# Kernel tuning notes

Measured on AMD Instinct MI355X. Metric: run time of the kernel, lower is better.

The kernel has to match this reference:

```python
import jax, jax.numpy as jnp
import numpy as np

N_NODES = 100000
N_EDGES = 3200000
D_FEAT = 256
FILTERS = 256


def setup_inputs() -> dict:
    key = jax.random.key(0)
    k1, k2, k3, k4, k5 = jax.random.split(key, 5)
    x = jax.random.normal(k1, (N_NODES, D_FEAT), dtype=jnp.float32)
    edge_row = jax.random.randint(k2, (N_EDGES,), 0, N_NODES, dtype=jnp.int32)
    edge_col = jax.random.randint(k3, (N_EDGES,), 0, N_NODES, dtype=jnp.int32)
    edge_vals = jnp.ones((N_EDGES,), dtype=jnp.float32)
    w = jax.random.normal(k4, (D_FEAT, FILTERS), dtype=jnp.float32) * (2.0 / D_FEAT) ** 0.5  # he_normal
    b = jax.random.normal(k5, (FILTERS,), dtype=jnp.float32) * 0.05
    return {"x": x, "edge_row": edge_row, "edge_col": edge_col,
            "edge_vals": edge_vals, "w": w, "b": b}


def reference(x, edge_row, edge_col, edge_vals, w, b):
    n = x.shape[0]
    # normalize_A: D = rowsum(A); L = D^{-1/2} A D^{-1/2}
    deg = jax.ops.segment_sum(edge_vals, edge_row, num_segments=n)
    dinv = jnp.where(deg > 0, deg ** -0.5, 0.0)  # [N]
    norm_vals = edge_vals * dinv[edge_row] * dinv[edge_col]  # [E]
    # dense projection then sparse aggregation + bias + relu
    h = x @ w  # [N, F]
    msg = norm_vals[:, None] * h[edge_col]  # [E, F] gather + scale
    agg = jax.ops.segment_sum(msg, edge_row, num_segments=n)  # [N, F]
    return jax.nn.relu(agg + b)
```

## Files before the change

### kernel.cpp

```cpp
#include <hip/hip_runtime.h>
#include <hip/hip_bf16.h>


#define DF   256
#define RSH  7
#define RPB  128
#define CAP  4800
#define CHUNK 8192
#define LSTR 40

typedef __attribute__((ext_vector_type(8))) short short8;
typedef __attribute__((ext_vector_type(4))) float f32x4;

__device__ __forceinline__ unsigned short f2bf(float f) {
    unsigned int u = __float_as_uint(f);
    unsigned int r = (u + 0x7fffu + ((u >> 16) & 1u)) >> 16;
    return (unsigned short)r;
}
__device__ __forceinline__ unsigned int pack2(float a, float b) {
    unsigned int r;
    asm("v_cvt_pk_bf16_f32 %0, %1, %2" : "=v"(r) : "v"(a), "v"(b));
    return r;
}
__device__ __forceinline__ float bflo(unsigned int u) { return __uint_as_float(u << 16); }
__device__ __forceinline__ float bfhi(unsigned int u) { return __uint_as_float(u & 0xffff0000u); }

__global__ __launch_bounds__(256) void bhist_kernel(const int* __restrict__ row,
                                                    int* __restrict__ bh1, int NB, int NBLK, int E) {
    __shared__ int hist[1024];
    int t = threadIdx.x;
    for (int i = t; i < NB; i += 256) hist[i] = 0;
    __syncthreads();
    int base = blockIdx.x * CHUNK;
    int end = base + CHUNK; if (end > E) end = E;
    for (int i = base + t; i < end; i += 256)
        atomicAdd(&hist[row[i] >> RSH], 1);
    __syncthreads();
    for (int i = t; i < NB; i += 256)
        bh1[(size_t)i * NBLK + blockIdx.x] = hist[i];
}

__global__ __launch_bounds__(256) void bscan_kernel(const int* __restrict__ bh1,
                                                    int* __restrict__ bh2,
                                                    int* __restrict__ buckettot, int NB, int NBLK) {
    __shared__ int ps[256];
    int b = blockIdx.x, t = threadIdx.x;
    int e0 = 2 * t, e1 = 2 * t + 1;
    int v0 = (e0 < NBLK) ? bh1[(size_t)b * NBLK + e0] : 0;
    int v1 = (e1 < NBLK) ? bh1[(size_t)b * NBLK + e1] : 0;
    int tsum = v0 + v1;
    ps[t] = tsum;
    __syncthreads();
    for (int off = 1; off < 256; off <<= 1) {
        int v = (t >= off) ? ps[t - off] : 0;
        __syncthreads();
        ps[t] += v;
        __syncthreads();
    }
    int pre = ps[t] - tsum;
    if (e0 < NBLK) bh2[(size_t)e0 * NB + b] = pre;
    if (e1 < NBLK) bh2[(size_t)e1 * NB + b] = pre + v0;
    if (t == 255) buckettot[b] = ps[255];
}

__global__ __launch_bounds__(1024) void btot_kernel(const int* __restrict__ buckettot,
                                                    int* __restrict__ bucket_base, int NB) {
    __shared__ int ps[1024];
    int t = threadIdx.x;
    int v = (t < NB) ? buckettot[t] : 0;
    ps[t] = v;
    __syncthreads();
    for (int off = 1; off < 1024; off <<= 1) {
        int u = (t >= off) ? ps[t - off] : 0;
        __syncthreads();
        ps[t] += u;
        __syncthreads();
    }
    if (t < NB) bucket_base[t] = ps[t] - v;
    if (t == 1023) bucket_base[NB] = ps[1023];
}

__global__ __launch_bounds__(512) void bsort_kernel(const int* __restrict__ row,
                                                    const int* __restrict__ col,
                                                    const float* __restrict__ vals,
                                                    const int* __restrict__ bh2,
                                                    const int* __restrict__ bucket_base,
                                                    int2* __restrict__ bedge, int NB, int E) {
    __shared__ int2 sedge[CHUNK];
    __shared__ unsigned short sbkt[CHUNK];
    __shared__ int lhist[1024];
    __shared__ int lscan[1024];
    __shared__ int lbase[1024];
    __shared__ int ps[512];
    int t = threadIdx.x, blk = blockIdx.x;
    int base = blk * CHUNK;
    int end = base + CHUNK; if (end > E) end = E;
    int n = end - base;
    for (int i = t; i < NB; i += 512) {
        lhist[i] = 0;
        lbase[i] = bucket_base[i] + bh2[(size_t)blk * NB + i];
    }
    __syncthreads();
    for (int i = base + t; i < end; i += 512)
        atomicAdd(&lhist[row[i] >> RSH], 1);
    __syncthreads();
    int e0 = 2 * t, e1 = 2 * t + 1;
    int v0 = (e0 < NB) ? lhist[e0] : 0;
    int v1 = (e1 < NB) ? lhist[e1] : 0;
    int tsum = v0 + v1;
    ps[t] = tsum;
    __syncthreads();
    for (int off = 1; off < 512; off <<= 1) {
        int v = (t >= off) ? ps[t - off] : 0;
        __syncthreads();
        ps[t] += v;
        __syncthreads();
    }
    int pre = ps[t] - tsum;
    if (e0 < NB) lscan[e0] = pre;
    if (e1 < NB) lscan[e1] = pre + v0;
    __syncthreads();
    for (int i = t; i < NB; i += 512) lhist[i] = 0;
    __syncthreads();
    for (int i = base + t; i < end; i += 512) {
        int r = row[i];
        int b = r >> RSH;
        int p = atomicAdd(&lhist[b], 1);
        int slot = lscan[b] + p;
        sedge[slot] = make_int2(((r & (RPB - 1)) << 17) | col[i], __float_as_int(vals[i]));
        sbkt[slot] = (unsigned short)b;
    }
    __syncthreads();
    for (int i = t; i < n; i += 512) {
        int b = sbkt[i];
        bedge[lbase[b] + (i - lscan[b])] = sedge[i];
    }
}

__global__ __launch_bounds__(256) void deg_kernel(const int2* __restrict__ bedge,
                                                  const int* __restrict__ bucket_base,
                                                  float* __restrict__ dinv, int N) {
    __shared__ float acc[RPB];
    int b = blockIdx.x, t = threadIdx.x;
    if (t < RPB) acc[t] = 0.f;
    __syncthreads();
    int s = bucket_base[b], e = bucket_base[b + 1];
    for (int i = s + t; i < e; i += 256) {
        int2 ed = bedge[i];
        atomicAdd(&acc[ed.x >> 17], __int_as_float(ed.y));
    }
    __syncthreads();
    if (t < RPB) {
        int r = b * RPB + t;
        if (r < N) {
            float d = acc[t];
            dinv[r] = (d > 0.f) ? (1.0f / sqrtf(d)) : 0.f;
        }
    }
}

__global__ __launch_bounds__(256) void transpose_kernel(const float* __restrict__ w,
                                                        float* __restrict__ wT) {
    __shared__ float tile[32][33];
    int bx = blockIdx.x * 32, by = blockIdx.y * 32;
    int tx = threadIdx.x, ty = threadIdx.y;
    for (int j = ty; j < 32; j += 8) tile[j][tx] = w[(by + j) * DF + bx + tx];
    __syncthreads();
    for (int j = ty; j < 32; j += 8) wT[(bx + j) * DF + by + tx] = tile[tx][j];
}

__global__ __launch_bounds__(256, 2) void gemm_kernel(const float* __restrict__ x,
                                                      const float* __restrict__ wT,
                                                      const float* __restrict__ dinv,
                                                      unsigned short* __restrict__ h, int N) {
    __shared__ unsigned short Al[128 * LSTR];
    __shared__ unsigned short Bl[256 * LSTR];
    int tid = threadIdx.x;
    int by = blockIdx.x;
    int wv = tid >> 6, lane = tid & 63;
    int wr = wv >> 1, wc = wv & 1;
    int q = lane >> 4, mi = lane & 15;

    f32x4 acc[4][8];
#pragma unroll
    for (int i = 0; i < 4; ++i)
#pragma unroll
        for (int j = 0; j < 8; ++j) acc[i][j] = (f32x4){0.f, 0.f, 0.f, 0.f};

    int srow = tid >> 1;
    int sseg = (tid & 1) * 16;
    int axrow = by * 128 + srow; if (axrow >= N) axrow = N - 1;
    const float* ax = x + (long)axrow * DF + sseg;
    const float* bxp = wT + (long)tid * DF;
    unsigned short* Aw = &Al[srow * LSTR + sseg];
    unsigned short* Bw = &Bl[tid * LSTR];

    for (int kk = 0; kk < DF; kk += 32) {
        float4 a0 = *(const float4*)(ax + kk);
        float4 a1 = *(const float4*)(ax + kk + 4);
        float4 a2 = *(const float4*)(ax + kk + 8);
        float4 a3 = *(const float4*)(ax + kk + 12);
        float4 b0 = *(const float4*)(bxp + kk);
        float4 b1 = *(const float4*)(bxp + kk + 4);
        float4 b2 = *(const float4*)(bxp + kk + 8);
        float4 b3 = *(const float4*)(bxp + kk + 12);
        float4 b4 = *(const float4*)(bxp + kk + 16);
        float4 b5 = *(const float4*)(bxp + kk + 20);
        float4 b6 = *(const float4*)(bxp + kk + 24);
        float4 b7 = *(const float4*)(bxp + kk + 28);
        __syncthreads();
        uint4 pa;
        pa.x = pack2(a0.x, a0.y); pa.y = pack2(a0.z, a0.w);
        pa.z = pack2(a1.x, a1.y); pa.w = pack2(a1.z, a1.w);
        *(uint4*)Aw = pa;
        pa.x = pack2(a2.x, a2.y); pa.y = pack2(a2.z, a2.w);
        pa.z = pack2(a3.x, a3.y); pa.w = pack2(a3.z, a3.w);
        *(uint4*)(Aw + 8) = pa;
        uint4 pb;
        pb.x = pack2(b0.x, b0.y); pb.y = pack2(b0.z, b0.w);
        pb.z = pack2(b1.x, b1.y); pb.w = pack2(b1.z, b1.w);
        *(uint4*)Bw = pb;
        pb.x = pack2(b2.x, b2.y); pb.y = pack2(b2.z, b2.w);
        pb.z = pack2(b3.x, b3.y); pb.w = pack2(b3.z, b3.w);
        *(uint4*)(Bw + 8) = pb;
        pb.x = pack2(b4.x, b4.y); pb.y = pack2(b4.z, b4.w);
        pb.z = pack2(b5.x, b5.y); pb.w = pack2(b5.z, b5.w);
        *(uint4*)(Bw + 16) = pb;
        pb.x = pack2(b6.x, b6.y); pb.y = pack2(b6.z, b6.w);
        pb.z = pack2(b7.x, b7.y); pb.w = pack2(b7.z, b7.w);
        *(uint4*)(Bw + 24) = pb;
        __syncthreads();

        short8 af[4];
#pragma unroll
        for (int i = 0; i < 4; ++i)
            af[i] = *(const short8*)&Al[(wr * 64 + i * 16 + mi) * LSTR + q * 8];
#pragma unroll
        for (int j = 0; j < 8; ++j) {
            short8 bfj = *(const short8*)&Bl[(wc * 128 + j * 16 + mi) * LSTR + q * 8];
#pragma unroll
            for (int i = 0; i < 4; ++i)
                acc[i][j] = __builtin_amdgcn_mfma_f32_16x16x32_bf16(af[i], bfj, acc[i][j], 0, 0, 0);
        }
    }

#pragma unroll
    for (int i = 0; i < 4; ++i) {
        int base_row = by * 128 + wr * 64 + i * 16 + q * 4;
#pragma unroll
        for (int r = 0; r < 4; ++r) {
            int rg = base_row + r;
            if (rg < N) {
                float dv = dinv[rg];
#pragma unroll
                for (int j = 0; j < 8; ++j) {
                    int cg = wc * 128 + j * 16 + mi;
                    h[(long)rg * DF + cg] = f2bf(dv * acc[i][j][r]);
                }
            }
        }
    }
}

__global__ __launch_bounds__(256) void aggb_kernel(const unsigned short* __restrict__ h,
                                                   const int2* __restrict__ bedge,
                                                   const int* __restrict__ bucket_base,
                                                   const float* __restrict__ dinv,
                                                   const float* __restrict__ bias,
                                                   float* __restrict__ out, int N) {
    __shared__ int2 ledge[CAP];
    __shared__ int cnt[RPB];
    __shared__ int lrs[RPB + 1];
    __shared__ int lfill[RPB];
    int b = blockIdx.x, t = threadIdx.x;
    int s = bucket_base[b], e = bucket_base[b + 1];
    int tot = e - s;
    int cap_end = s + (tot < CAP ? tot : CAP);
    if (t < RPB) { cnt[t] = 0; lfill[t] = 0; }
    __syncthreads();
    for (int i = s + t; i < cap_end; i += 256)
        atomicAdd(&cnt[bedge[i].x >> 17], 1);
    __syncthreads();
    int myc = 0;
    if (t < RPB) { myc = cnt[t]; lrs[t] = myc; }
    __syncthreads();
    for (int off = 1; off < RPB; off <<= 1) {
        int v = (t < RPB && t >= off) ? lrs[t - off] : 0;
        __syncthreads();
        if (t < RPB) lrs[t] += v;
        __syncthreads();
    }
    if (t < RPB) {
        int iv = lrs[t];
        lrs[t] = iv - myc;
        if (t == RPB - 1) lrs[RPB] = iv;
    }
    __syncthreads();
    for (int i = s + t; i < cap_end; i += 256) {
        int2 ed = bedge[i];
        int rl = ed.x >> 17;
        int p = lrs[rl] + atomicAdd(&lfill[rl], 1);
        ledge[p] = make_int2(ed.x & 0x1FFFF, ed.y);
    }
    __syncthreads();
    int wv = t >> 6, lane = t & 63;
    int half = lane >> 5;
    int fl = (lane & 31) * 8;
    const unsigned short* hp = h + fl;
    for (int lr = wv; lr < RPB; lr += 4) {
        int r = b * RPB + lr;
        if (r >= N) break;
        int rs = lrs[lr], re = lrs[lr + 1];
        float a0 = 0, a1 = 0, a2 = 0, a3 = 0, a4 = 0, a5 = 0, a6 = 0, a7 = 0;
        int i = rs + half;
        for (; i + 6 < re; i += 8) {
            int2 e0 = ledge[i], e1 = ledge[i + 2], e2 = ledge[i + 4], e3 = ledge[i + 6];
            uint4 u0 = *(const uint4*)(hp + (long)e0.x * DF);
            uint4 u1 = *(const uint4*)(hp + (long)e1.x * DF);
            uint4 u2 = *(const uint4*)(hp + (long)e2.x * DF);
            uint4 u3 = *(const uint4*)(hp + (long)e3.x * DF);
            float v0 = __int_as_float(e0.y), v1 = __int_as_float(e1.y);
            float v2 = __int_as_float(e2.y), v3 = __int_as_float(e3.y);
            a0 += v0 * bflo(u0.x) + v1 * bflo(u1.x) + v2 * bflo(u2.x) + v3 * bflo(u3.x);
            a1 += v0 * bfhi(u0.x) + v1 * bfhi(u1.x) + v2 * bfhi(u2.x) + v3 * bfhi(u3.x);
            a2 += v0 * bflo(u0.y) + v1 * bflo(u1.y) + v2 * bflo(u2.y) + v3 * bflo(u3.y);
            a3 += v0 * bfhi(u0.y) + v1 * bfhi(u1.y) + v2 * bfhi(u2.y) + v3 * bfhi(u3.y);
            a4 += v0 * bflo(u0.z) + v1 * bflo(u1.z) + v2 * bflo(u2.z) + v3 * bflo(u3.z);
            a5 += v0 * bfhi(u0.z) + v1 * bfhi(u1.z) + v2 * bfhi(u2.z) + v3 * bfhi(u3.z);
            a6 += v0 * bflo(u0.w) + v1 * bflo(u1.w) + v2 * bflo(u2.w) + v3 * bflo(u3.w);
            a7 += v0 * bfhi(u0.w) + v1 * bfhi(u1.w) + v2 * bfhi(u2.w) + v3 * bfhi(u3.w);
        }
        for (; i < re; i += 2) {
            int2 e0 = ledge[i];
            float v0 = __int_as_float(e0.y);
            uint4 u0 = *(const uint4*)(hp + (long)e0.x * DF);
            a0 += v0 * bflo(u0.x); a1 += v0 * bfhi(u0.x);
            a2 += v0 * bflo(u0.y); a3 += v0 * bfhi(u0.y);
            a4 += v0 * bflo(u0.z); a5 += v0 * bfhi(u0.z);
            a6 += v0 * bflo(u0.w); a7 += v0 * bfhi(u0.w);
        }
        for (int j = cap_end + half; j < e; j += 2) {
            int2 ed = bedge[j];
            if ((ed.x >> 17) == lr) {
                float v0 = __int_as_float(ed.y);
                uint4 u0 = *(const uint4*)(hp + (long)(ed.x & 0x1FFFF) * DF);
                a0 += v0 * bflo(u0.x); a1 += v0 * bfhi(u0.x);
                a2 += v0 * bflo(u0.y); a3 += v0 * bfhi(u0.y);
                a4 += v0 * bflo(u0.z); a5 += v0 * bfhi(u0.z);
                a6 += v0 * bflo(u0.w); a7 += v0 * bfhi(u0.w);
            }
        }
        a0 += __shfl_xor(a0, 32); a1 += __shfl_xor(a1, 32);
        a2 += __shfl_xor(a2, 32); a3 += __shfl_xor(a3, 32);
        a4 += __shfl_xor(a4, 32); a5 += __shfl_xor(a5, 32);
        a6 += __shfl_xor(a6, 32); a7 += __shfl_xor(a7, 32);
        if (half == 0) {
            float dr = dinv[r];
            float4 b0 = *(const float4*)(bias + fl);
            float4 b1 = *(const float4*)(bias + fl + 4);
            float4 o0, o1;
            o0.x = fmaxf(fmaf(dr, a0, b0.x), 0.f);
            o0.y = fmaxf(fmaf(dr, a1, b0.y), 0.f);
            o0.z = fmaxf(fmaf(dr, a2, b0.z), 0.f);
            o0.w = fmaxf(fmaf(dr, a3, b0.w), 0.f);
            o1.x = fmaxf(fmaf(dr, a4, b1.x), 0.f);
            o1.y = fmaxf(fmaf(dr, a5, b1.y), 0.f);
            o1.z = fmaxf(fmaf(dr, a6, b1.z), 0.f);
            o1.w = fmaxf(fmaf(dr, a7, b1.w), 0.f);
            *(float4*)(out + (long)r * DF + fl) = o0;
            *(float4*)(out + (long)r * DF + fl + 4) = o1;
        }
    }
}

extern "C" void kernel_launch(void* const* d_in, const int* in_sizes, int n_in,
                              void* d_out, int out_size, void* d_ws, size_t ws_size,
                              hipStream_t stream) {
    const float* x   = (const float*)d_in[0];
    const int* erow  = (const int*)d_in[1];
    const int* ecol  = (const int*)d_in[2];
    const float* ev  = (const float*)d_in[3];
    const float* w   = (const float*)d_in[4];
    const float* b   = (const float*)d_in[5];
    float* out = (float*)d_out;

    int N = in_sizes[0] / DF;
    int E = in_sizes[1];
    int NB = (N + RPB - 1) >> RSH;
    int NBLK = (E + CHUNK - 1) / CHUNK;

    char* ws = (char*)d_ws;
    size_t Ea8 = (((size_t)E * 8) + 255) & ~(size_t)255;
    size_t Hs  = (((size_t)N * DF * 2) + 255) & ~(size_t)255;
    size_t Na  = (((size_t)N * 4) + 255) & ~(size_t)255;

    int2* bedge = (int2*)ws;
    char* reg2 = ws + Ea8;
    unsigned short* h = (unsigned short*)reg2;
    int* bh1 = (int*)reg2;
    int* bh2 = bh1 + (size_t)NB * NBLK;
    char* reg3 = reg2 + Hs;
    float* wT = (float*)reg3;
    float* dinv = (float*)(reg3 + 262144);
    int* buckettot = (int*)(reg3 + 262144 + Na);
    int* bucket_base = (int*)(reg3 + 262144 + Na + 8192);

    bhist_kernel<<<NBLK, 256, 0, stream>>>(erow, bh1, NB, NBLK, E);
    bscan_kernel<<<NB, 256, 0, stream>>>(bh1, bh2, buckettot, NB, NBLK);
    btot_kernel<<<1, 1024, 0, stream>>>(buckettot, bucket_base, NB);
    bsort_kernel<<<NBLK, 512, 0, stream>>>(erow, ecol, ev, bh2, bucket_base, bedge, NB, E);
    deg_kernel<<<NB, 256, 0, stream>>>(bedge, bucket_base, dinv, N);
    transpose_kernel<<<dim3(8, 8), dim3(32, 8), 0, stream>>>(w, wT);
    gemm_kernel<<<dim3((N + 127) / 128), 256, 0, stream>>>(x, wT, dinv, h, N);
    aggb_kernel<<<NB, 256, 0, stream>>>(h, bedge, bucket_base, dinv, b, out, N);
}
```

Before: 590.7 us.

## Load GEMM operands directly into MFMA registers, pre-convert weights to bf16

The transpose kernel now writes the weight matrix as bf16, and the GEMM drops its LDS staging. Each lane loads its MFMA fragments straight from global memory and prefetches the next K-slice of x in registers. This removes the LDS writes and reads and both per-iteration barriers. In exchange, the x rows are loaded in a less coalesced pattern, and each wave reloads its weight fragments from L2/L1 rather than sharing them through LDS, which may raise cache traffic and register pressure.

```diff
diff --git a/kernel.cpp b/kernel.cpp
--- a/kernel.cpp
+++ b/kernel.cpp
@@ -7,7 +7,6 @@
 #define RPB  128
 #define CAP  4800
 #define CHUNK 8192
-#define LSTR 40
 
 typedef __attribute__((ext_vector_type(8))) short short8;
 typedef __attribute__((ext_vector_type(4))) float f32x4;
@@ -160,21 +159,19 @@
 }
 
 __global__ __launch_bounds__(256) void transpose_kernel(const float* __restrict__ w,
-                                                        float* __restrict__ wT) {
+                                                        unsigned short* __restrict__ wbT) {
     __shared__ float tile[32][33];
     int bx = blockIdx.x * 32, by = blockIdx.y * 32;
     int tx = threadIdx.x, ty = threadIdx.y;
     for (int j = ty; j < 32; j += 8) tile[j][tx] = w[(by + j) * DF + bx + tx];
     __syncthreads();
-    for (int j = ty; j < 32; j += 8) wT[(bx + j) * DF + by + tx] = tile[tx][j];
+    for (int j = ty; j < 32; j += 8) wbT[(bx + j) * DF + by + tx] = f2bf(tile[tx][j]);
 }
 
 __global__ __launch_bounds__(256, 2) void gemm_kernel(const float* __restrict__ x,
-                                                      const float* __restrict__ wT,
+                                                      const unsigned short* __restrict__ wbT,
                                                       const float* __restrict__ dinv,
                                                       unsigned short* __restrict__ h, int N) {
-    __shared__ unsigned short Al[128 * LSTR];
-    __shared__ unsigned short Bl[256 * LSTR];
     int tid = threadIdx.x;
     int by = blockIdx.x;
     int wv = tid >> 6, lane = tid & 63;
@@ -187,60 +184,64 @@
 #pragma unroll
         for (int j = 0; j < 8; ++j) acc[i][j] = (f32x4){0.f, 0.f, 0.f, 0.f};
 
-    int srow = tid >> 1;
-    int sseg = (tid & 1) * 16;
-    int axrow = by * 128 + srow; if (axrow >= N) axrow = N - 1;
-    const float* ax = x + (long)axrow * DF + sseg;
-    const float* bxp = wT + (long)tid * DF;
-    unsigned short* Aw = &Al[srow * LSTR + sseg];
-    unsigned short* Bw = &Bl[tid * LSTR];
-
-    for (int kk = 0; kk < DF; kk += 32) {
-        float4 a0 = *(const float4*)(ax + kk);
-        float4 a1 = *(const float4*)(ax + kk + 4);
-        float4 a2 = *(const float4*)(ax + kk + 8);
-        float4 a3 = *(const float4*)(ax + kk + 12);
-        float4 b0 = *(const float4*)(bxp + kk);
-        float4 b1 = *(const float4*)(bxp + kk + 4);
-        float4 b2 = *(const float4*)(bxp + kk + 8);
-        float4 b3 = *(const float4*)(bxp + kk + 12);
-        float4 b4 = *(const float4*)(bxp + kk + 16);
-        float4 b5 = *(const float4*)(bxp + kk + 20);
-        float4 b6 = *(const float4*)(bxp + kk + 24);
-        float4 b7 = *(const float4*)(bxp + kk + 28);
-        __syncthreads();
-        uint4 pa;
-        pa.x = pack2(a0.x, a0.y); pa.y = pack2(a0.z, a0.w);
-        pa.z = pack2(a1.x, a1.y); pa.w = pack2(a1.z, a1.w);
-        *(uint4*)Aw = pa;
-        pa.x = pack2(a2.x, a2.y); pa.y = pack2(a2.z, a2.w);
-        pa.z = pack2(a3.x, a3.y); pa.w = pack2(a3.z, a3.w);
-        *(uint4*)(Aw + 8) = pa;
-        uint4 pb;
-        pb.x = pack2(b0.x, b0.y); pb.y = pack2(b0.z, b0.w);
-        pb.z = pack2(b1.x, b1.y); pb.w = pack2(b1.z, b1.w);
-        *(uint4*)Bw = pb;
-        pb.x = pack2(b2.x, b2.y); pb.y = pack2(b2.z, b2.w);
-        pb.z = pack2(b3.x, b3.y); pb.w = pack2(b3.z, b3.w);
-        *(uint4*)(Bw + 8) = pb;
-        pb.x = pack2(b4.x, b4.y); pb.y = pack2(b4.z, b4.w);
-        pb.z = pack2(b5.x, b5.y); pb.w = pack2(b5.z, b5.w);
-        *(uint4*)(Bw + 16) = pb;
-        pb.x = pack2(b6.x, b6.y); pb.y = pack2(b6.z, b6.w);
-        pb.z = pack2(b7.x, b7.y); pb.w = pack2(b7.z, b7.w);
-        *(uint4*)(Bw + 24) = pb;
-        __syncthreads();
-
-        short8 af[4];
-#pragma unroll
-        for (int i = 0; i < 4; ++i)
-            af[i] = *(const short8*)&Al[(wr * 64 + i * 16 + mi) * LSTR + q * 8];
+    const float* axp[4];
+#pragma unroll
+    for (int i = 0; i < 4; ++i) {
+        int r = by * 128 + wr * 64 + i * 16 + mi;
+        if (r >= N) r = N - 1;
+        axp[i] = x + (long)r * DF + q * 8;
+    }
+    const unsigned short* bwp[8];
+#pragma unroll
+    for (int j = 0; j < 8; ++j)
+        bwp[j] = wbT + (long)(wc * 128 + j * 16 + mi) * DF + q * 8;
+
+    short8 af[4];
+    {
+        float4 p0[4], p1[4];
+#pragma unroll
+        for (int i = 0; i < 4; ++i) {
+            p0[i] = *(const float4*)(axp[i]);
+            p1[i] = *(const float4*)(axp[i] + 4);
+        }
+#pragma unroll
+        for (int i = 0; i < 4; ++i) {
+            uint4 pk;
+            pk.x = pack2(p0[i].x, p0[i].y); pk.y = pack2(p0[i].z, p0[i].w);
+            pk.z = pack2(p1[i].x, p1[i].y); pk.w = pack2(p1[i].z, p1[i].w);
+            af[i] = *(short8*)&pk;
+        }
+    }
+
+    for (int t = 0; t < 8; ++t) {
+        int kk = t * 32;
+        uint4 bw[8];
+#pragma unroll
+        for (int j = 0; j < 8; ++j)
+            bw[j] = *(const uint4*)(bwp[j] + kk);
+        float4 n0[4], n1[4];
+        if (t < 7) {
+#pragma unroll
+            for (int i = 0; i < 4; ++i) {
+                n0[i] = *(const float4*)(axp[i] + kk + 32);
+                n1[i] = *(const float4*)(axp[i] + kk + 36);
+            }
+        }
 #pragma unroll
         for (int j = 0; j < 8; ++j) {
-            short8 bfj = *(const short8*)&Bl[(wc * 128 + j * 16 + mi) * LSTR + q * 8];
+            short8 bfj = *(short8*)&bw[j];
 #pragma unroll
             for (int i = 0; i < 4; ++i)
                 acc[i][j] = __builtin_amdgcn_mfma_f32_16x16x32_bf16(af[i], bfj, acc[i][j], 0, 0, 0);
+        }
+        if (t < 7) {
+#pragma unroll
+            for (int i = 0; i < 4; ++i) {
+                uint4 pk;
+                pk.x = pack2(n0[i].x, n0[i].y); pk.y = pack2(n0[i].z, n0[i].w);
+                pk.z = pack2(n1[i].x, n1[i].y); pk.w = pack2(n1[i].z, n1[i].w);
+                af[i] = *(short8*)&pk;
+            }
         }
     }
 
@@ -400,7 +401,7 @@
     int* bh1 = (int*)reg2;
     int* bh2 = bh1 + (size_t)NB * NBLK;
     char* reg3 = reg2 + Hs;
-    float* wT = (float*)reg3;
+    unsigned short* wbT = (unsigned short*)reg3;
     float* dinv = (float*)(reg3 + 262144);
     int* buckettot = (int*)(reg3 + 262144 + Na);
     int* bucket_base = (int*)(reg3 + 262144 + Na + 8192);
@@ -410,7 +411,7 @@
     btot_kernel<<<1, 1024, 0, stream>>>(buckettot, bucket_base, NB);
     bsort_kernel<<<NBLK, 512, 0, stream>>>(erow, ecol, ev, bh2, bucket_base, bedge, NB, E);
     deg_kernel<<<NB, 256, 0, stream>>>(bedge, bucket_base, dinv, N);
-    transpose_kernel<<<dim3(8, 8), dim3(32, 8), 0, stream>>>(w, wT);
-    gemm_kernel<<<dim3((N + 127) / 128), 256, 0, stream>>>(x, wT, dinv, h, N);
+    transpose_kernel<<<dim3(8, 8), dim3(32, 8), 0, stream>>>(w, wbT);
+    gemm_kernel<<<dim3((N + 127) / 128), 256, 0, stream>>>(x, wbT, dinv, h, N);
     aggb_kernel<<<NB, 256, 0, stream>>>(h, bedge, bucket_base, dinv, b, out, N);
 }
```

Result: no change. 589.2 us (-0.2%).
